# Kernel optimization log

Hardware: AMD Instinct MI355X
Metric: run time of the kernel (lower is better)

The kernel has to match this reference:

```python
import jax, jax.numpy as jnp
import numpy as np

NEG = -1e9


def setup_inputs() -> dict:
    key = jax.random.key(0)
    kq, kk, kv, ke = jax.random.split(key, 4)
    B, H, S, D = 4, 16, 2048, 64
    q = jax.random.normal(kq, (B, H, S, D), dtype=jnp.float32)
    k = jax.random.normal(kk, (B, H, S, D), dtype=jnp.float32)
    v = jax.random.normal(kv, (B, H, S, D), dtype=jnp.float32)
    event_length = jax.random.randint(ke, (B,), 0, S, dtype=jnp.int32)
    return {"q": q, "k": k, "v": v, "event_length": event_length}


def reference(q, k, v, event_length):
    B, H, S, D = q.shape
    scale = jnp.sqrt(jnp.asarray(D, dtype=jnp.float32))
    # [b,h,s,q] scores
    scores = jnp.einsum('bhsd,bhqd->bhsq', q, k) / scale
    idx = jnp.arange(S)
    el = event_length[:, None]  # [B,1]
    valid = idx[None, :] < el   # [B,S]
    # mask[b,s,q] = valid[b,s] & valid[b,q]; broadcast over heads
    mask = (valid[:, None, :, None] & valid[:, None, None, :])  # [B,1,S,S]
    scores = jnp.where(mask, scores, NEG)
    attn = jax.nn.softmax(scores, axis=-1)
    # dropout p=0.0 (eval): identity
    out = jnp.einsum('bhsq,bhqd->bhsd', attn, v)
    return out
```

## Files before the change

kernel.cpp:

```cpp
#include <hip/hip_runtime.h>
#include <hip/hip_bf16.h>


#define SQ 2048
#define DH 64
#define NBH 64
#define TK 64
#define NTILE 32
#define TILE_B 8192
#define PH_B 16384
#define LDE 72
#define LVP 68

typedef __attribute__((ext_vector_type(4))) float f32x4;
typedef __attribute__((ext_vector_type(8))) short bf16x8;
typedef __attribute__((ext_vector_type(4))) unsigned int u32x4;
typedef __attribute__((ext_vector_type(2))) unsigned int u32x2;

#define VMCNT(n) asm volatile("s_waitcnt vmcnt(" #n ")" ::: "memory")
#define RAW_BARRIER() asm volatile("s_barrier" ::: "memory")

__device__ __forceinline__ unsigned int pk2(float lo, float hi) {
    __hip_bfloat162 h = __float22bfloat162_rn(float2{lo, hi});
    union { __hip_bfloat162 h; unsigned int u; } c; c.h = h;
    return c.u;
}

__device__ __forceinline__ float bfu16_to_f(unsigned short s) {
    union { unsigned int u; float f; } c; c.u = ((unsigned int)s) << 16;
    return c.f;
}

__device__ __forceinline__ void async_cp16(const void* g, void* l) {
    __builtin_amdgcn_global_load_lds(
        (const __attribute__((address_space(1))) unsigned int*)g,
        (__attribute__((address_space(3))) unsigned int*)l, 16, 0, 0);
}


__global__ __launch_bounds__(256)
void convkv(const float* __restrict__ K, const float* __restrict__ V,
            const int* __restrict__ EL, float* __restrict__ MV,
            char* __restrict__ Kbt, char* __restrict__ Vbt) {
    const int bh = blockIdx.x >> 5;
    const int kt = blockIdx.x & 31;
    const int k0 = kt * TK;
    const int el = EL[bh >> 4];
    const int t = threadIdx.x;
    const int r  = t >> 2;
    const int dc = t & 3;

    __shared__ short LV[64][LVP];

    {
        const float* vp = V + ((size_t)bh * SQ + k0 + r) * DH + dc * 16;
        f32x4 a = *(const f32x4*)vp;
        f32x4 b = *(const f32x4*)(vp + 4);
        f32x4 c2 = *(const f32x4*)(vp + 8);
        f32x4 d2 = *(const f32x4*)(vp + 12);
        u32x4 w0, w1;
        w0[0] = pk2(a[0], a[1]);  w0[1] = pk2(a[2], a[3]);
        w0[2] = pk2(b[0], b[1]);  w0[3] = pk2(b[2], b[3]);
        w1[0] = pk2(c2[0], c2[1]); w1[1] = pk2(c2[2], c2[3]);
        w1[2] = pk2(d2[0], d2[1]); w1[3] = pk2(d2[2], d2[3]);
        *(u32x4*)&LV[r][dc * 16]     = w0;
        *(u32x4*)&LV[r][dc * 16 + 8] = w1;
    }

    if (k0 < el) {
        const float* kp = K + ((size_t)bh * SQ + k0 + r) * DH + dc * 16;
        f32x4 a = *(const f32x4*)kp;
        f32x4 b = *(const f32x4*)(kp + 4);
        f32x4 c2 = *(const f32x4*)(kp + 8);
        f32x4 d2 = *(const f32x4*)(kp + 12);
        u32x4 w0, w1;
        w0[0] = pk2(a[0], a[1]);  w0[1] = pk2(a[2], a[3]);
        w0[2] = pk2(b[0], b[1]);  w0[3] = pk2(b[2], b[3]);
        w1[0] = pk2(c2[0], c2[1]); w1[1] = pk2(c2[2], c2[3]);
        w1[2] = pk2(d2[0], d2[1]); w1[3] = pk2(d2[2], d2[3]);
        char* kb = Kbt + (size_t)(bh * NTILE + kt) * TILE_B;
        const int fi  = (r >> 4) * 2 + (dc >> 1);
        const int qd0 = (dc & 1) * 2;
        char* d0 = kb + fi * 1024 + qd0 * 256 + (r & 15) * 16;
        *(u32x4*)d0         = w0;
        *(u32x4*)(d0 + 256) = w1;
    }

    __syncthreads();

    const int dd  = t >> 2;
    const int seg = t & 3;
    float msum = 0.f;
    unsigned int wv[8];
    #pragma unroll
    for (int i = 0; i < 8; ++i) {
        const int pos = seg * 16 + 2 * i;
        const int key = (pos & ~31) | ((pos & 4) << 2) | ((pos & 24) >> 1) | (pos & 3);
        const unsigned short s0 = (unsigned short)LV[key][dd];
        const unsigned short s1 = (unsigned short)LV[key + 1][dd];
        msum += bfu16_to_f(s0) + bfu16_to_f(s1);
        wv[i] = (unsigned int)s0 | ((unsigned int)s1 << 16);
    }
    msum += __shfl_xor(msum, 1);
    msum += __shfl_xor(msum, 2);
    if (seg == 0) atomicAdd(&MV[bh * DH + dd], msum * (1.0f / (float)SQ));

    if (k0 < el) {
        char* vbb = Vbt + (size_t)(bh * NTILE + kt) * TILE_B;
        const int fi  = (seg >> 1) * 4 + (dd >> 4);
        const int qd0 = (seg & 1) * 2;
        char* d0 = vbb + fi * 1024 + qd0 * 256 + (dd & 15) * 16;
        u32x4 o0 = {wv[0], wv[1], wv[2], wv[3]};
        u32x4 o1 = {wv[4], wv[5], wv[6], wv[7]};
        *(u32x4*)d0         = o0;
        *(u32x4*)(d0 + 256) = o1;
    }
}

__global__ __launch_bounds__(512, 4)
void flash15(const float* __restrict__ Q, const int* __restrict__ EL,
             const float* __restrict__ MV, float* __restrict__ O,
             const char* __restrict__ Kbt, const char* __restrict__ Vbt) {
    const int t = threadIdx.x;

    {
        const int bh0 = blockIdx.x & (NBH - 1);
        const int qb0 = (blockIdx.x >> 6) * 256;
        const int elb = EL[bh0 >> 4];
        if (qb0 >= elb) {
            float* Op = O + (size_t)bh0 * SQ * DH;
            const int c16 = t & 15, r0 = t >> 4;
            f32x4 mv = *(const f32x4*)(MV + bh0 * DH + c16 * 4);
            #pragma unroll
            for (int i = 0; i < 8; ++i)
                *(f32x4*)(Op + (size_t)(qb0 + r0 + i * 32) * DH + c16 * 4) = mv;
        }
    }

    int ka0 = EL[0], va0 = 0;
    int ka1 = EL[1], va1 = 1;
    int ka2 = EL[2], va2 = 2;
    int ka3 = EL[3], va3 = 3;
    #define CSWAP(x, y) if (ka##x < ka##y) { int tk_ = ka##x, tv_ = va##x; \
        ka##x = ka##y; va##x = va##y; ka##y = tk_; va##y = tv_; }
    CSWAP(0, 1) CSWAP(2, 3) CSWAP(0, 2) CSWAP(1, 3) CSWAP(1, 2)
    #undef CSWAP
    const int c0 = 2 * ((ka0 + 255) >> 8);
    const int c1 = 2 * ((ka1 + 255) >> 8);
    const int c2 = 2 * ((ka2 + 255) >> 8);
    const int c3 = 2 * ((ka3 + 255) >> 8);
    const int nvalid = c0 + c1 + c2 + c3;

    __shared__ char KB[2 * PH_B];
    __shared__ char VB[2 * PH_B];

    const int grp = blockIdx.x & 7;
    const int it  = blockIdx.x >> 3;
    if (it >= nvalid) return;

    int u = it, b, el;
    if (u < c0)             { b = va0; el = ka0; }
    else { u -= c0;
    if (u < c1)             { b = va1; el = ka1; }
    else { u -= c1;
    if (u < c2)             { b = va2; el = ka2; }
    else { u -= c2;           b = va3; el = ka3; } } }
    const int vb_ = (el + 255) >> 8;
    const int hh  = u / vb_;
    const int qt  = u - hh * vb_;
    const int bh  = b * 16 + grp + hh * 8;
    const int qbase = qt * 256;

    const int wq = t >> 6, lane = t & 63, qd = lane >> 4, c = lane & 15;
    const float sc = 0.125f * 1.44269504f;

    const float* Qp = Q + (size_t)bh * SQ * DH;
    float*       Op = O + (size_t)bh * SQ * DH;
    const char*  Kt = Kbt + (size_t)bh * NTILE * TILE_B + t * 16;
    const char*  Vt = Vbt + (size_t)bh * NTILE * TILE_B + t * 16;

    const int nph = (el + 127) >> 7;

    #define STAGE(ph_, s_) {                                                   \
        const char* gk_ = Kt + (size_t)(ph_) * PH_B;                           \
        const char* gv_ = Vt + (size_t)(ph_) * PH_B;                           \
        char* lk_ = KB + (s_) * PH_B + t * 16;                                 \
        char* lv_ = VB + (s_) * PH_B + t * 16;                                 \
        async_cp16(gk_,        lk_);                                           \
        async_cp16(gk_ + 8192, lk_ + 8192);                                    \
        async_cp16(gv_,        lv_);                                           \
        async_cp16(gv_ + 8192, lv_ + 8192);                                    \
    }

    STAGE(0, 0)

    bf16x8 qf[2][2];
    #pragma unroll
    for (int nt = 0; nt < 2; ++nt) {
        const int row = qbase + wq * 32 + nt * 16 + c;
        #pragma unroll
        for (int kc = 0; kc < 2; ++kc) {
            const float* p = Qp + (size_t)row * DH + kc * 32 + qd * 8;
            f32x4 a  = *(const f32x4*)p;
            f32x4 bq = *(const f32x4*)(p + 4);
            u32x4 f;
            f[0] = pk2(a[0] * sc, a[1] * sc);
            f[1] = pk2(a[2] * sc, a[3] * sc);
            f[2] = pk2(bq[0] * sc, bq[1] * sc);
            f[3] = pk2(bq[2] * sc, bq[3] * sc);
            qf[nt][kc] = *(bf16x8*)&f;
        }
    }

    float l_[2] = {0.f, 0.f};
    f32x4 oacc[4][2];
    #pragma unroll
    for (int dt = 0; dt < 4; ++dt) {
        oacc[dt][0] = (f32x4){0.f, 0.f, 0.f, 0.f};
        oacc[dt][1] = (f32x4){0.f, 0.f, 0.f, 0.f};
    }

    for (int ph = 0; ph < nph; ++ph) {
        const int s = ph & 1;

        RAW_BARRIER();
        if (ph + 1 < nph) STAGE(ph + 1, s ^ 1)
        if (ph + 1 < nph) VMCNT(4); else VMCNT(0);
        RAW_BARRIER();

        #pragma unroll
        for (int su = 0; su < 2; ++su) {
            const int k0 = ph * 128 + su * 64;
            if (k0 >= el) break;

            const char* Kb = KB + s * PH_B + su * TILE_B + lane * 16;
            const char* Vb = VB + s * PH_B + su * TILE_B + lane * 16;

            f32x4 st[4][2];
            __builtin_amdgcn_s_setprio(1);
            #pragma unroll
            for (int mt = 0; mt < 4; ++mt) {
                bf16x8 a0 = *(const bf16x8*)(Kb + (mt * 2) * 1024);
                bf16x8 a1 = *(const bf16x8*)(Kb + (mt * 2 + 1) * 1024);
                #pragma unroll
                for (int nt = 0; nt < 2; ++nt) {
                    f32x4 acc = (f32x4){0.f, 0.f, 0.f, 0.f};
                    acc = __builtin_amdgcn_mfma_f32_16x16x32_bf16(a0, qf[nt][0], acc, 0, 0, 0);
                    acc = __builtin_amdgcn_mfma_f32_16x16x32_bf16(a1, qf[nt][1], acc, 0, 0, 0);
                    st[mt][nt] = acc;
                }
            }
            __builtin_amdgcn_s_setprio(0);

            if (k0 + TK > el) {
                #pragma unroll
                for (int mt = 0; mt < 4; ++mt)
                    #pragma unroll
                    for (int r = 0; r < 4; ++r)
                        if (k0 + mt * 16 + qd * 4 + r >= el) {
                            st[mt][0][r] = -1e30f;
                            st[mt][1][r] = -1e30f;
                        }
            }

            u32x4 pw[2][2];
            #pragma unroll
            for (int nt = 0; nt < 2; ++nt) {
                #pragma unroll
                for (int mt = 0; mt < 4; ++mt) {
                    const float p0 = __builtin_amdgcn_exp2f(st[mt][nt][0]);
                    const float p1 = __builtin_amdgcn_exp2f(st[mt][nt][1]);
                    const float p2 = __builtin_amdgcn_exp2f(st[mt][nt][2]);
                    const float p3 = __builtin_amdgcn_exp2f(st[mt][nt][3]);
                    l_[nt] += (p0 + p1) + (p2 + p3);
                    pw[nt][mt >> 1][(mt & 1) * 2]     = pk2(p0, p1);
                    pw[nt][mt >> 1][(mt & 1) * 2 + 1] = pk2(p2, p3);
                }
            }

            __builtin_amdgcn_s_setprio(1);
            #pragma unroll
            for (int kc = 0; kc < 2; ++kc) {
                bf16x8 pb0 = *(bf16x8*)&pw[0][kc];
                bf16x8 pb1 = *(bf16x8*)&pw[1][kc];
                #pragma unroll
                for (int dt = 0; dt < 4; ++dt) {
                    bf16x8 vf = *(const bf16x8*)(Vb + (kc * 4 + dt) * 1024);
                    oacc[dt][0] = __builtin_amdgcn_mfma_f32_16x16x32_bf16(vf, pb0, oacc[dt][0], 0, 0, 0);
                    oacc[dt][1] = __builtin_amdgcn_mfma_f32_16x16x32_bf16(vf, pb1, oacc[dt][1], 0, 0, 0);
                }
            }
            __builtin_amdgcn_s_setprio(0);
        }
    }
    #undef STAGE

    #pragma unroll
    for (int nt = 0; nt < 2; ++nt) {
        l_[nt] += __shfl_xor(l_[nt], 16);
        l_[nt] += __shfl_xor(l_[nt], 32);
    }

    #pragma unroll
    for (int nt = 0; nt < 2; ++nt) {
        const int qrow = qbase + wq * 32 + nt * 16 + c;
        if (qrow < el) {
            const float inv = 1.0f / l_[nt];
            #pragma unroll
            for (int dt = 0; dt < 4; ++dt) {
                f32x4 o = oacc[dt][nt];
                o[0] *= inv; o[1] *= inv; o[2] *= inv; o[3] *= inv;
                *(f32x4*)(Op + (size_t)qrow * DH + dt * 16 + qd * 4) = o;
            }
        } else {
            #pragma unroll
            for (int dt = 0; dt < 4; ++dt)
                *(f32x4*)(Op + (size_t)qrow * DH + dt * 16 + qd * 4) =
                    *(const f32x4*)(MV + bh * DH + dt * 16 + qd * 4);
        }
    }
}


__global__ __launch_bounds__(256)
void meanv_k(const float* __restrict__ V, float* __restrict__ MV) {
    const int bh  = blockIdx.x >> 4;
    const int seg = blockIdx.x & 15;
    const float* vp = V + ((size_t)bh * SQ + (size_t)seg * 128) * DH;
    const int c = threadIdx.x & 15;
    const int r = threadIdx.x >> 4;
    const float* p = vp + (size_t)r * DH + c * 4;
    f32x4 s0 = *(const f32x4*)(p);
    f32x4 s1 = *(const f32x4*)(p + 16 * DH);
    f32x4 s2 = *(const f32x4*)(p + 32 * DH);
    f32x4 s3 = *(const f32x4*)(p + 48 * DH);
    s0 += *(const f32x4*)(p + 64 * DH);
    s1 += *(const f32x4*)(p + 80 * DH);
    s2 += *(const f32x4*)(p + 96 * DH);
    s3 += *(const f32x4*)(p + 112 * DH);
    f32x4 s = (s0 + s1) + (s2 + s3);
    __shared__ f32x4 red[16][16];
    red[r][c] = s;
    __syncthreads();
    if (threadIdx.x < 16) {
        f32x4 a = red[0][threadIdx.x];
        #pragma unroll
        for (int j = 1; j < 16; ++j) a += red[j][threadIdx.x];
        const float inv = 1.0f / (float)SQ;
        atomicAdd(&MV[bh * DH + threadIdx.x * 4 + 0], a[0] * inv);
        atomicAdd(&MV[bh * DH + threadIdx.x * 4 + 1], a[1] * inv);
        atomicAdd(&MV[bh * DH + threadIdx.x * 4 + 2], a[2] * inv);
        atomicAdd(&MV[bh * DH + threadIdx.x * 4 + 3], a[3] * inv);
    }
}

__global__ __launch_bounds__(256, 3)
void flash5(const float* __restrict__ Q, const float* __restrict__ K,
            const float* __restrict__ V, const int* __restrict__ EL,
            const float* __restrict__ MV, float* __restrict__ O,
            int* __restrict__ ticket) {
    const int t = threadIdx.x;
    {
        const int bh0    = blockIdx.x & (NBH - 1);
        const int qbase0 = (blockIdx.x >> 6) * 128;
        const int elb    = EL[bh0 >> 4];
        if (qbase0 >= elb) {
            float* Op = O + (size_t)bh0 * SQ * DH;
            const int c16 = t & 15, r0 = t >> 4;
            f32x4 mv = *(const f32x4*)(MV + bh0 * DH + c16 * 4);
            #pragma unroll
            for (int i = 0; i < 8; ++i)
                *(f32x4*)(Op + (size_t)(qbase0 + r0 + i * 16) * DH + c16 * 4) = mv;
        }
    }

    const int el0 = EL[0], el1 = EL[1], el2 = EL[2], el3 = EL[3];
    const int v0 = (el0 + 127) >> 7, v1 = (el1 + 127) >> 7;
    const int v2 = (el2 + 127) >> 7, v3 = (el3 + 127) >> 7;
    const int n0 = 16 * v0, n1 = n0 + 16 * v1, n2 = n1 + 16 * v2;
    const int nvalid = n2 + 16 * v3;

    __shared__ short Kb[TK][LDE];
    __shared__ short Vt[DH][LDE];
    __shared__ short Pl[4][32][LDE];
    __shared__ int item_s;

    const int wq = t >> 6, lane = t & 63, qd = lane >> 4, c = lane & 15;
    const int ksrow = t >> 2;
    const int ksdc  = t & 3;
    const int vpair = t & 31;
    const int vdg   = t >> 5;

    for (;;) {
        if (t == 0) item_s = atomicAdd(ticket, 1);
        __syncthreads();
        const int it = item_s;
        if (it >= nvalid) break;

        int b, u, vb, el;
        if      (it < n0) { b = 0; u = it;      vb = v0; el = el0; }
        else if (it < n1) { b = 1; u = it - n0; vb = v1; el = el1; }
        else if (it < n2) { b = 2; u = it - n1; vb = v2; el = el2; }
        else              { b = 3; u = it - n2; vb = v3; el = el3; }
        const int head  = u / vb;
        const int qt    = u - head * vb;
        const int bh    = b * 16 + head;
        const int qbase = qt * 128;

        const size_t base = (size_t)bh * SQ * DH;
        const float* Qp = Q + base;
        const float* Kp = K + base;
        const float* Vp = V + base;
        float* Op = O + base;

        const float sc = 0.125f * 1.44269504f;
        bf16x8 qf[2][2];
        #pragma unroll
        for (int nt = 0; nt < 2; ++nt) {
            const int row = qbase + wq * 32 + nt * 16 + c;
            #pragma unroll
            for (int kc = 0; kc < 2; ++kc) {
                const float* p = Qp + (size_t)row * DH + kc * 32 + qd * 8;
                f32x4 a  = *(const f32x4*)p;
                f32x4 bb = *(const f32x4*)(p + 4);
                u32x4 f;
                f[0] = pk2(a[0] * sc, a[1] * sc);
                f[1] = pk2(a[2] * sc, a[3] * sc);
                f[2] = pk2(bb[0] * sc, bb[1] * sc);
                f[3] = pk2(bb[2] * sc, bb[3] * sc);
                qf[nt][kc] = *(bf16x8*)&f;
            }
        }

        float l_[2] = {0.f, 0.f};
        f32x4 oacc[4][2];
        #pragma unroll
        for (int dt = 0; dt < 4; ++dt)
            #pragma unroll
            for (int nt = 0; nt < 2; ++nt)
                oacc[dt][nt] = (f32x4){0.f, 0.f, 0.f, 0.f};

        const int nkt = (el + TK - 1) / TK;

        f32x4 kg0, kg1, kg2, kg3, vg0, vg1, vg2, vg3;
        {
            const float* kp = Kp + (size_t)ksrow * DH + ksdc * 16;
            kg0 = *(const f32x4*)kp;
            kg1 = *(const f32x4*)(kp + 4);
            kg2 = *(const f32x4*)(kp + 8);
            kg3 = *(const f32x4*)(kp + 12);
            const float* vp0 = Vp + (size_t)(2 * vpair) * DH + vdg * 8;
            vg0 = *(const f32x4*)vp0;
            vg1 = *(const f32x4*)(vp0 + 4);
            vg2 = *(const f32x4*)(vp0 + DH);
            vg3 = *(const f32x4*)(vp0 + DH + 4);
        }

        for (int kt = 0; kt < nkt; ++kt) {
            const int k0 = kt * TK;

            __syncthreads();
            {
                u32x4 w0, w1;
                w0[0] = pk2(kg0[0], kg0[1]); w0[1] = pk2(kg0[2], kg0[3]);
                w0[2] = pk2(kg1[0], kg1[1]); w0[3] = pk2(kg1[2], kg1[3]);
                w1[0] = pk2(kg2[0], kg2[1]); w1[1] = pk2(kg2[2], kg2[3]);
                w1[2] = pk2(kg3[0], kg3[1]); w1[3] = pk2(kg3[2], kg3[3]);
                *(u32x4*)&Kb[ksrow][ksdc * 16]     = w0;
                *(u32x4*)&Kb[ksrow][ksdc * 16 + 8] = w1;
            }
            {
                #pragma unroll
                for (int i = 0; i < 4; ++i) {
                    *(unsigned int*)&Vt[vdg * 8 + i][2 * vpair]     = pk2(vg0[i], vg2[i]);
                    *(unsigned int*)&Vt[vdg * 8 + 4 + i][2 * vpair] = pk2(vg1[i], vg3[i]);
                }
            }
            __syncthreads();

            if (kt + 1 < nkt) {
                const int kn = k0 + TK;
                const float* kp = Kp + (size_t)(kn + ksrow) * DH + ksdc * 16;
                kg0 = *(const f32x4*)kp;
                kg1 = *(const f32x4*)(kp + 4);
                kg2 = *(const f32x4*)(kp + 8);
                kg3 = *(const f32x4*)(kp + 12);
                const float* vp0 = Vp + (size_t)(kn + 2 * vpair) * DH + vdg * 8;
                vg0 = *(const f32x4*)vp0;
                vg1 = *(const f32x4*)(vp0 + 4);
                vg2 = *(const f32x4*)(vp0 + DH);
                vg3 = *(const f32x4*)(vp0 + DH + 4);
            }

            f32x4 st[4][2];
            #pragma unroll
            for (int mt = 0; mt < 4; ++mt) {
                bf16x8 a0 = *(const bf16x8*)&Kb[mt * 16 + c][qd * 8];
                bf16x8 a1 = *(const bf16x8*)&Kb[mt * 16 + c][32 + qd * 8];
                #pragma unroll
                for (int nt = 0; nt < 2; ++nt) {
                    f32x4 acc = (f32x4){0.f, 0.f, 0.f, 0.f};
                    acc = __builtin_amdgcn_mfma_f32_16x16x32_bf16(a0, qf[nt][0], acc, 0, 0, 0);
                    acc = __builtin_amdgcn_mfma_f32_16x16x32_bf16(a1, qf[nt][1], acc, 0, 0, 0);
                    st[mt][nt] = acc;
                }
            }

            if (k0 + TK > el) {
                #pragma unroll
                for (int mt = 0; mt < 4; ++mt)
                    #pragma unroll
                    for (int r = 0; r < 4; ++r)
                        if (k0 + mt * 16 + qd * 4 + r >= el) {
                            st[mt][0][r] = -1e30f;
                            st[mt][1][r] = -1e30f;
                        }
            }

            #pragma unroll
            for (int nt = 0; nt < 2; ++nt) {
                #pragma unroll
                for (int mt = 0; mt < 4; ++mt) {
                    const float p0 = exp2f(st[mt][nt][0]);
                    const float p1 = exp2f(st[mt][nt][1]);
                    const float p2 = exp2f(st[mt][nt][2]);
                    const float p3 = exp2f(st[mt][nt][3]);
                    l_[nt] += (p0 + p1) + (p2 + p3);
                    u32x2 pw;
                    pw[0] = pk2(p0, p1);
                    pw[1] = pk2(p2, p3);
                    *(u32x2*)&Pl[wq][nt * 16 + c][mt * 16 + qd * 4] = pw;
                }
            }

            #pragma unroll
            for (int kc = 0; kc < 2; ++kc) {
                bf16x8 pb0 = *(const bf16x8*)&Pl[wq][c][kc * 32 + qd * 8];
                bf16x8 pb1 = *(const bf16x8*)&Pl[wq][16 + c][kc * 32 + qd * 8];
                #pragma unroll
                for (int dt = 0; dt < 4; ++dt) {
                    bf16x8 vf = *(const bf16x8*)&Vt[dt * 16 + c][kc * 32 + qd * 8];
                    oacc[dt][0] = __builtin_amdgcn_mfma_f32_16x16x32_bf16(vf, pb0, oacc[dt][0], 0, 0, 0);
                    oacc[dt][1] = __builtin_amdgcn_mfma_f32_16x16x32_bf16(vf, pb1, oacc[dt][1], 0, 0, 0);
                }
            }
        }

        #pragma unroll
        for (int nt = 0; nt < 2; ++nt) {
            l_[nt] += __shfl_xor(l_[nt], 16);
            l_[nt] += __shfl_xor(l_[nt], 32);
        }

        #pragma unroll
        for (int nt = 0; nt < 2; ++nt) {
            const int row = qbase + wq * 32 + nt * 16 + c;
            if (row < el) {
                const float inv = 1.0f / l_[nt];
                #pragma unroll
                for (int dt = 0; dt < 4; ++dt) {
                    f32x4 o = oacc[dt][nt];
                    o[0] *= inv; o[1] *= inv; o[2] *= inv; o[3] *= inv;
                    *(f32x4*)(Op + (size_t)row * DH + dt * 16 + qd * 4) = o;
                }
            } else {
                #pragma unroll
                for (int dt = 0; dt < 4; ++dt) {
                    f32x4 mv = *(const f32x4*)(MV + bh * DH + dt * 16 + qd * 4);
                    *(f32x4*)(Op + (size_t)row * DH + dt * 16 + qd * 4) = mv;
                }
            }
        }
    }
}


extern "C" void kernel_launch(void* const* d_in, const int* in_sizes, int n_in,
                              void* d_out, int out_size, void* d_ws, size_t ws_size,
                              hipStream_t stream) {
    const float* q  = (const float*)d_in[0];
    const float* k  = (const float*)d_in[1];
    const float* v  = (const float*)d_in[2];
    const int*   el = (const int*)d_in[3];
    float* out = (float*)d_out;

    const size_t kbt_bytes = (size_t)NBH * NTILE * TILE_B;
    const size_t needed    = 65536 + 2 * kbt_bytes;

    if (ws_size >= needed) {
        float* mv  = (float*)d_ws;
        char*  kbt = (char*)d_ws + 65536;
        char*  vbt = kbt + kbt_bytes;

        hipMemsetAsync(d_ws, 0, 65536, stream);
        convkv<<<dim3(NBH * NTILE), dim3(256), 0, stream>>>(k, v, el, mv, kbt, vbt);
        flash15<<<dim3(NBH * (SQ / 256)), dim3(512), 0, stream>>>(q, el, mv, out, kbt, vbt);
    } else {
        float* mv = (float*)d_ws;
        int*   tk = (int*)((char*)d_ws + NBH * DH * sizeof(float));

        hipMemsetAsync(d_ws, 0, NBH * DH * sizeof(float) + 64, stream);
        meanv_k<<<dim3(NBH * 16), dim3(256), 0, stream>>>(v, mv);
        flash5<<<dim3(NBH * (SQ / 128)), dim3(256), 0, stream>>>(q, k, v, el, mv, out, tk);
    }
}
```

Before: 186.1 us.

## Halve block to 256 threads with 64 query rows per wave

Each workgroup now has 4 waves instead of 8, and each wave handles 64 query rows instead of 32. Every K/V fragment loaded from LDS therefore feeds twice as many MFMAs, and fewer waves share each staged K/V tile. The score computation, masking and exp2 are also fused per 16x16 tile so the full score array is never held at once. The cost is a larger accumulator and register footprint (16 output accumulators per lane), lower occupancy (launch bounds 2), and fewer waves available to hide latency.

```diff
diff --git a/kernel.cpp b/kernel.cpp
--- a/kernel.cpp
+++ b/kernel.cpp
@@ -117,8 +117,8 @@
     }
 }
 
-__global__ __launch_bounds__(512, 4)
-void flash15(const float* __restrict__ Q, const int* __restrict__ EL,
+__global__ __launch_bounds__(256, 2)
+void flash17(const float* __restrict__ Q, const int* __restrict__ EL,
              const float* __restrict__ MV, float* __restrict__ O,
              const char* __restrict__ Kbt, const char* __restrict__ Vbt) {
     const int t = threadIdx.x;
@@ -132,8 +132,8 @@
             const int c16 = t & 15, r0 = t >> 4;
             f32x4 mv = *(const f32x4*)(MV + bh0 * DH + c16 * 4);
             #pragma unroll
-            for (int i = 0; i < 8; ++i)
-                *(f32x4*)(Op + (size_t)(qb0 + r0 + i * 32) * DH + c16 * 4) = mv;
+            for (int i = 0; i < 16; ++i)
+                *(f32x4*)(Op + (size_t)(qb0 + r0 + i * 16) * DH + c16 * 4) = mv;
         }
     }
 
@@ -186,18 +186,19 @@
         const char* gv_ = Vt + (size_t)(ph_) * PH_B;                           \
         char* lk_ = KB + (s_) * PH_B + t * 16;                                 \
         char* lv_ = VB + (s_) * PH_B + t * 16;                                 \
-        async_cp16(gk_,        lk_);                                           \
-        async_cp16(gk_ + 8192, lk_ + 8192);                                    \
-        async_cp16(gv_,        lv_);                                           \
-        async_cp16(gv_ + 8192, lv_ + 8192);                                    \
+        _Pragma("unroll")                                                      \
+        for (int j_ = 0; j_ < 4; ++j_) {                                       \
+            async_cp16(gk_ + j_ * 4096, lk_ + j_ * 4096);                      \
+            async_cp16(gv_ + j_ * 4096, lv_ + j_ * 4096);                      \
+        }                                                                      \
     }
 
     STAGE(0, 0)
 
-    bf16x8 qf[2][2];
+    bf16x8 qf[4][2];
     #pragma unroll
-    for (int nt = 0; nt < 2; ++nt) {
-        const int row = qbase + wq * 32 + nt * 16 + c;
+    for (int nt = 0; nt < 4; ++nt) {
+        const int row = qbase + wq * 64 + nt * 16 + c;
         #pragma unroll
         for (int kc = 0; kc < 2; ++kc) {
             const float* p = Qp + (size_t)row * DH + kc * 32 + qd * 8;
@@ -212,20 +213,20 @@
         }
     }
 
-    float l_[2] = {0.f, 0.f};
-    f32x4 oacc[4][2];
+    float l_[4] = {0.f, 0.f, 0.f, 0.f};
+    f32x4 oacc[4][4];
     #pragma unroll
-    for (int dt = 0; dt < 4; ++dt) {
-        oacc[dt][0] = (f32x4){0.f, 0.f, 0.f, 0.f};
-        oacc[dt][1] = (f32x4){0.f, 0.f, 0.f, 0.f};
-    }
+    for (int dt = 0; dt < 4; ++dt)
+        #pragma unroll
+        for (int nt = 0; nt < 4; ++nt)
+            oacc[dt][nt] = (f32x4){0.f, 0.f, 0.f, 0.f};
 
     for (int ph = 0; ph < nph; ++ph) {
         const int s = ph & 1;
 
         RAW_BARRIER();
         if (ph + 1 < nph) STAGE(ph + 1, s ^ 1)
-        if (ph + 1 < nph) VMCNT(4); else VMCNT(0);
+        if (ph + 1 < nph) VMCNT(8); else VMCNT(0);
         RAW_BARRIER();
 
         #pragma unroll
@@ -235,43 +236,29 @@
 
             const char* Kb = KB + s * PH_B + su * TILE_B + lane * 16;
             const char* Vb = VB + s * PH_B + su * TILE_B + lane * 16;
-
-            f32x4 st[4][2];
-            __builtin_amdgcn_s_setprio(1);
+            const bool strad = (k0 + TK > el);
+
+            u32x4 pw[4][2];
             #pragma unroll
             for (int mt = 0; mt < 4; ++mt) {
                 bf16x8 a0 = *(const bf16x8*)(Kb + (mt * 2) * 1024);
                 bf16x8 a1 = *(const bf16x8*)(Kb + (mt * 2 + 1) * 1024);
                 #pragma unroll
-                for (int nt = 0; nt < 2; ++nt) {
-                    f32x4 acc = (f32x4){0.f, 0.f, 0.f, 0.f};
-                    acc = __builtin_amdgcn_mfma_f32_16x16x32_bf16(a0, qf[nt][0], acc, 0, 0, 0);
-                    acc = __builtin_amdgcn_mfma_f32_16x16x32_bf16(a1, qf[nt][1], acc, 0, 0, 0);
-                    st[mt][nt] = acc;
-                }
-            }
-            __builtin_amdgcn_s_setprio(0);
-
-            if (k0 + TK > el) {
-                #pragma unroll
-                for (int mt = 0; mt < 4; ++mt)
-                    #pragma unroll
-                    for (int r = 0; r < 4; ++r)
-                        if (k0 + mt * 16 + qd * 4 + r >= el) {
-                            st[mt][0][r] = -1e30f;
-                            st[mt][1][r] = -1e30f;
-                        }
-            }
-
-            u32x4 pw[2][2];
-            #pragma unroll
-            for (int nt = 0; nt < 2; ++nt) {
-                #pragma unroll
-                for (int mt = 0; mt < 4; ++mt) {
-                    const float p0 = __builtin_amdgcn_exp2f(st[mt][nt][0]);
-                    const float p1 = __builtin_amdgcn_exp2f(st[mt][nt][1]);
-                    const float p2 = __builtin_amdgcn_exp2f(st[mt][nt][2]);
-                    const float p3 = __builtin_amdgcn_exp2f(st[mt][nt][3]);
+                for (int nt = 0; nt < 4; ++nt) {
+                    f32x4 sv = (f32x4){0.f, 0.f, 0.f, 0.f};
+                    __builtin_amdgcn_s_setprio(1);
+                    sv = __builtin_amdgcn_mfma_f32_16x16x32_bf16(a0, qf[nt][0], sv, 0, 0, 0);
+                    sv = __builtin_amdgcn_mfma_f32_16x16x32_bf16(a1, qf[nt][1], sv, 0, 0, 0);
+                    __builtin_amdgcn_s_setprio(0);
+                    if (strad) {
+                        #pragma unroll
+                        for (int r = 0; r < 4; ++r)
+                            if (k0 + mt * 16 + qd * 4 + r >= el) sv[r] = -1e30f;
+                    }
+                    const float p0 = __builtin_amdgcn_exp2f(sv[0]);
+                    const float p1 = __builtin_amdgcn_exp2f(sv[1]);
+                    const float p2 = __builtin_amdgcn_exp2f(sv[2]);
+                    const float p3 = __builtin_amdgcn_exp2f(sv[3]);
                     l_[nt] += (p0 + p1) + (p2 + p3);
                     pw[nt][mt >> 1][(mt & 1) * 2]     = pk2(p0, p1);
                     pw[nt][mt >> 1][(mt & 1) * 2 + 1] = pk2(p2, p3);
@@ -281,13 +268,14 @@
             __builtin_amdgcn_s_setprio(1);
             #pragma unroll
             for (int kc = 0; kc < 2; ++kc) {
-                bf16x8 pb0 = *(bf16x8*)&pw[0][kc];
-                bf16x8 pb1 = *(bf16x8*)&pw[1][kc];
                 #pragma unroll
                 for (int dt = 0; dt < 4; ++dt) {
                     bf16x8 vf = *(const bf16x8*)(Vb + (kc * 4 + dt) * 1024);
-                    oacc[dt][0] = __builtin_amdgcn_mfma_f32_16x16x32_bf16(vf, pb0, oacc[dt][0], 0, 0, 0);
-                    oacc[dt][1] = __builtin_amdgcn_mfma_f32_16x16x32_bf16(vf, pb1, oacc[dt][1], 0, 0, 0);
+                    #pragma unroll
+                    for (int nt = 0; nt < 4; ++nt) {
+                        bf16x8 pb = *(bf16x8*)&pw[nt][kc];
+                        oacc[dt][nt] = __builtin_amdgcn_mfma_f32_16x16x32_bf16(vf, pb, oacc[dt][nt], 0, 0, 0);
+                    }
                 }
             }
             __builtin_amdgcn_s_setprio(0);
@@ -296,14 +284,14 @@
     #undef STAGE
 
     #pragma unroll
-    for (int nt = 0; nt < 2; ++nt) {
+    for (int nt = 0; nt < 4; ++nt) {
         l_[nt] += __shfl_xor(l_[nt], 16);
         l_[nt] += __shfl_xor(l_[nt], 32);
     }
 
     #pragma unroll
-    for (int nt = 0; nt < 2; ++nt) {
-        const int qrow = qbase + wq * 32 + nt * 16 + c;
+    for (int nt = 0; nt < 4; ++nt) {
+        const int qrow = qbase + wq * 64 + nt * 16 + c;
         if (qrow < el) {
             const float inv = 1.0f / l_[nt];
             #pragma unroll
@@ -594,7 +582,7 @@
 
         hipMemsetAsync(d_ws, 0, 65536, stream);
         convkv<<<dim3(NBH * NTILE), dim3(256), 0, stream>>>(k, v, el, mv, kbt, vbt);
-        flash15<<<dim3(NBH * (SQ / 256)), dim3(512), 0, stream>>>(q, el, mv, out, kbt, vbt);
+        flash17<<<dim3(NBH * (SQ / 256)), dim3(256), 0, stream>>>(q, el, mv, out, kbt, vbt);
     } else {
         float* mv = (float*)d_ws;
         int*   tk = (int*)((char*)d_ws + NBH * DH * sizeof(float));
```

After: 192.9 us. +3.6%, slower.

## Split attention key range across blocks with atomic accumulation and finalize pass

Applied to the files above, without the earlier changes.

Adds a flash18 kernel that divides each query tile's key range into segments of 8 key tiles, each handled by its own block. When there are several segments, blocks add unnormalised outputs and row sums into the zeroed output and a workspace buffer using atomics. A new finalize kernel then normalises the rows and fills masked rows with the mean of V. The aim is more parallelism and better load balance across blocks when the valid lengths differ. The cost is a memset of the whole output, per-element float atomics, and an extra full read and write of the output.

```diff
diff --git a/kernel.cpp b/kernel.cpp
--- a/kernel.cpp
+++ b/kernel.cpp
@@ -9,6 +9,7 @@
 #define NTILE 32
 #define TILE_B 8192
 #define PH_B 16384
+#define PHSEG 8
 #define LDE 72
 #define LVP 68
 
@@ -36,7 +37,6 @@
         (const __attribute__((address_space(1))) unsigned int*)g,
         (__attribute__((address_space(3))) unsigned int*)l, 16, 0, 0);
 }
-
 
 __global__ __launch_bounds__(256)
 void convkv(const float* __restrict__ K, const float* __restrict__ V,
@@ -118,24 +118,13 @@
 }
 
 __global__ __launch_bounds__(512, 4)
-void flash15(const float* __restrict__ Q, const int* __restrict__ EL,
-             const float* __restrict__ MV, float* __restrict__ O,
+void flash18(const float* __restrict__ Q, const int* __restrict__ EL,
+             float* __restrict__ O, float* __restrict__ Lacc,
              const char* __restrict__ Kbt, const char* __restrict__ Vbt) {
-    const int t = threadIdx.x;
-
-    {
-        const int bh0 = blockIdx.x & (NBH - 1);
-        const int qb0 = (blockIdx.x >> 6) * 256;
-        const int elb = EL[bh0 >> 4];
-        if (qb0 >= elb) {
-            float* Op = O + (size_t)bh0 * SQ * DH;
-            const int c16 = t & 15, r0 = t >> 4;
-            f32x4 mv = *(const f32x4*)(MV + bh0 * DH + c16 * 4);
-            #pragma unroll
-            for (int i = 0; i < 8; ++i)
-                *(f32x4*)(Op + (size_t)(qb0 + r0 + i * 32) * DH + c16 * 4) = mv;
-        }
-    }
+    const int blk = blockIdx.x;
+    const int grp = blk & 7;
+    const int it  = (blk >> 3) & 63;
+    const int sgi = blk >> 9;
 
     int ka0 = EL[0], va0 = 0;
     int ka1 = EL[1], va1 = 1;
@@ -150,12 +139,6 @@
     const int c2 = 2 * ((ka2 + 255) >> 8);
     const int c3 = 2 * ((ka3 + 255) >> 8);
     const int nvalid = c0 + c1 + c2 + c3;
-
-    __shared__ char KB[2 * PH_B];
-    __shared__ char VB[2 * PH_B];
-
-    const int grp = blockIdx.x & 7;
-    const int it  = blockIdx.x >> 3;
     if (it >= nvalid) return;
 
     int u = it, b, el;
@@ -171,6 +154,16 @@
     const int bh  = b * 16 + grp + hh * 8;
     const int qbase = qt * 256;
 
+    const int nph  = (el + 63) >> 6;
+    const int nseg = (nph + PHSEG - 1) / PHSEG;
+    if (sgi >= nseg) return;
+    const int p0 = sgi * PHSEG;
+    const int p1 = (p0 + PHSEG < nph) ? p0 + PHSEG : nph;
+
+    __shared__ char KB[2 * TILE_B];
+    __shared__ char VB[2 * TILE_B];
+
+    const int t = threadIdx.x;
     const int wq = t >> 6, lane = t & 63, qd = lane >> 4, c = lane & 15;
     const float sc = 0.125f * 1.44269504f;
 
@@ -178,21 +171,15 @@
     float*       Op = O + (size_t)bh * SQ * DH;
     const char*  Kt = Kbt + (size_t)bh * NTILE * TILE_B + t * 16;
     const char*  Vt = Vbt + (size_t)bh * NTILE * TILE_B + t * 16;
-
-    const int nph = (el + 127) >> 7;
+    char* const  kdst = KB + wq * 1024;
+    char* const  vdst = VB + wq * 1024;
 
     #define STAGE(ph_, s_) {                                                   \
-        const char* gk_ = Kt + (size_t)(ph_) * PH_B;                           \
-        const char* gv_ = Vt + (size_t)(ph_) * PH_B;                           \
-        char* lk_ = KB + (s_) * PH_B + t * 16;                                 \
-        char* lv_ = VB + (s_) * PH_B + t * 16;                                 \
-        async_cp16(gk_,        lk_);                                           \
-        async_cp16(gk_ + 8192, lk_ + 8192);                                    \
-        async_cp16(gv_,        lv_);                                           \
-        async_cp16(gv_ + 8192, lv_ + 8192);                                    \
-    }
-
-    STAGE(0, 0)
+        async_cp16(Kt + (size_t)(ph_) * TILE_B, kdst + (s_) * TILE_B);         \
+        async_cp16(Vt + (size_t)(ph_) * TILE_B, vdst + (s_) * TILE_B);         \
+    }
+
+    STAGE(p0, 0)
 
     bf16x8 qf[2][2];
     #pragma unroll
@@ -220,9 +207,246 @@
         oacc[dt][1] = (f32x4){0.f, 0.f, 0.f, 0.f};
     }
 
+    for (int ph = p0; ph < p1; ++ph) {
+        const int s = (ph - p0) & 1;
+
+        RAW_BARRIER();
+        if (ph + 1 < p1) STAGE(ph + 1, s ^ 1)
+        if (ph + 1 < p1) VMCNT(2); else VMCNT(0);
+        RAW_BARRIER();
+
+        const char* Kb = KB + s * TILE_B + lane * 16;
+        const char* Vb = VB + s * TILE_B + lane * 16;
+
+        f32x4 st[4][2];
+        __builtin_amdgcn_s_setprio(1);
+        #pragma unroll
+        for (int mt = 0; mt < 4; ++mt) {
+            bf16x8 a0 = *(const bf16x8*)(Kb + (mt * 2) * 1024);
+            bf16x8 a1 = *(const bf16x8*)(Kb + (mt * 2 + 1) * 1024);
+            #pragma unroll
+            for (int nt = 0; nt < 2; ++nt) {
+                f32x4 acc = (f32x4){0.f, 0.f, 0.f, 0.f};
+                acc = __builtin_amdgcn_mfma_f32_16x16x32_bf16(a0, qf[nt][0], acc, 0, 0, 0);
+                acc = __builtin_amdgcn_mfma_f32_16x16x32_bf16(a1, qf[nt][1], acc, 0, 0, 0);
+                st[mt][nt] = acc;
+            }
+        }
+        __builtin_amdgcn_s_setprio(0);
+
+        const int k0 = ph * TK;
+        if (k0 + TK > el) {
+            #pragma unroll
+            for (int mt = 0; mt < 4; ++mt)
+                #pragma unroll
+                for (int r = 0; r < 4; ++r)
+                    if (k0 + mt * 16 + qd * 4 + r >= el) {
+                        st[mt][0][r] = -1e30f;
+                        st[mt][1][r] = -1e30f;
+                    }
+        }
+
+        u32x4 pw[2][2];
+        #pragma unroll
+        for (int nt = 0; nt < 2; ++nt) {
+            #pragma unroll
+            for (int mt = 0; mt < 4; ++mt) {
+                const float p0f = __builtin_amdgcn_exp2f(st[mt][nt][0]);
+                const float p1f = __builtin_amdgcn_exp2f(st[mt][nt][1]);
+                const float p2f = __builtin_amdgcn_exp2f(st[mt][nt][2]);
+                const float p3f = __builtin_amdgcn_exp2f(st[mt][nt][3]);
+                l_[nt] += (p0f + p1f) + (p2f + p3f);
+                pw[nt][mt >> 1][(mt & 1) * 2]     = pk2(p0f, p1f);
+                pw[nt][mt >> 1][(mt & 1) * 2 + 1] = pk2(p2f, p3f);
+            }
+        }
+
+        __builtin_amdgcn_s_setprio(1);
+        #pragma unroll
+        for (int kc = 0; kc < 2; ++kc) {
+            bf16x8 pb0 = *(bf16x8*)&pw[0][kc];
+            bf16x8 pb1 = *(bf16x8*)&pw[1][kc];
+            #pragma unroll
+            for (int dt = 0; dt < 4; ++dt) {
+                bf16x8 vf = *(const bf16x8*)(Vb + (kc * 4 + dt) * 1024);
+                oacc[dt][0] = __builtin_amdgcn_mfma_f32_16x16x32_bf16(vf, pb0, oacc[dt][0], 0, 0, 0);
+                oacc[dt][1] = __builtin_amdgcn_mfma_f32_16x16x32_bf16(vf, pb1, oacc[dt][1], 0, 0, 0);
+            }
+        }
+        __builtin_amdgcn_s_setprio(0);
+    }
+    #undef STAGE
+
+    #pragma unroll
+    for (int nt = 0; nt < 2; ++nt) {
+        l_[nt] += __shfl_xor(l_[nt], 16);
+        l_[nt] += __shfl_xor(l_[nt], 32);
+    }
+
+    if (nseg == 1) {
+        #pragma unroll
+        for (int nt = 0; nt < 2; ++nt) {
+            const int qrow = qbase + wq * 32 + nt * 16 + c;
+            if (qrow < el) {
+                const float inv = 1.0f / l_[nt];
+                #pragma unroll
+                for (int dt = 0; dt < 4; ++dt) {
+                    f32x4 o = oacc[dt][nt];
+                    o[0] *= inv; o[1] *= inv; o[2] *= inv; o[3] *= inv;
+                    *(f32x4*)(Op + (size_t)qrow * DH + dt * 16 + qd * 4) = o;
+                }
+            }
+        }
+    } else {
+        #pragma unroll
+        for (int nt = 0; nt < 2; ++nt) {
+            const int qrow = qbase + wq * 32 + nt * 16 + c;
+            if (qrow < el) {
+                float* op = Op + (size_t)qrow * DH + qd * 4;
+                #pragma unroll
+                for (int dt = 0; dt < 4; ++dt) {
+                    atomicAdd(op + dt * 16 + 0, oacc[dt][nt][0]);
+                    atomicAdd(op + dt * 16 + 1, oacc[dt][nt][1]);
+                    atomicAdd(op + dt * 16 + 2, oacc[dt][nt][2]);
+                    atomicAdd(op + dt * 16 + 3, oacc[dt][nt][3]);
+                }
+                if (qd == 0) atomicAdd(&Lacc[bh * SQ + qrow], l_[nt]);
+            }
+        }
+    }
+}
+
+__global__ __launch_bounds__(256)
+void finalize(const int* __restrict__ EL, const float* __restrict__ Lacc,
+              const float* __restrict__ MV, float* __restrict__ O) {
+    const int bh = blockIdx.x >> 4;
+    const int ch = blockIdx.x & 15;
+    const int el = EL[bh >> 4];
+    const int c16 = threadIdx.x & 15, r0 = threadIdx.x >> 4;
+    float* Op = O + (size_t)bh * SQ * DH;
+    const float* Lp = Lacc + bh * SQ;
+    f32x4 mv = *(const f32x4*)(MV + bh * DH + c16 * 4);
+    #pragma unroll
+    for (int i = 0; i < 8; ++i) {
+        const int row = ch * 128 + r0 + i * 16;
+        if (row >= el) {
+            *(f32x4*)(Op + (size_t)row * DH + c16 * 4) = mv;
+        } else {
+            const float l = Lp[row];
+            if (l != 0.f) {
+                const float inv = 1.0f / l;
+                f32x4 o = *(const f32x4*)(Op + (size_t)row * DH + c16 * 4);
+                o[0] *= inv; o[1] *= inv; o[2] *= inv; o[3] *= inv;
+                *(f32x4*)(Op + (size_t)row * DH + c16 * 4) = o;
+            }
+        }
+    }
+}
+
+__global__ __launch_bounds__(512, 4)
+void flash15(const float* __restrict__ Q, const int* __restrict__ EL,
+             const float* __restrict__ MV, float* __restrict__ O,
+             const char* __restrict__ Kbt, const char* __restrict__ Vbt) {
+    const int t = threadIdx.x;
+    {
+        const int bh0 = blockIdx.x & (NBH - 1);
+        const int qb0 = (blockIdx.x >> 6) * 256;
+        const int elb = EL[bh0 >> 4];
+        if (qb0 >= elb) {
+            float* Op = O + (size_t)bh0 * SQ * DH;
+            const int c16 = t & 15, r0 = t >> 4;
+            f32x4 mv = *(const f32x4*)(MV + bh0 * DH + c16 * 4);
+            #pragma unroll
+            for (int i = 0; i < 8; ++i)
+                *(f32x4*)(Op + (size_t)(qb0 + r0 + i * 32) * DH + c16 * 4) = mv;
+        }
+    }
+
+    int ka0 = EL[0], va0 = 0;
+    int ka1 = EL[1], va1 = 1;
+    int ka2 = EL[2], va2 = 2;
+    int ka3 = EL[3], va3 = 3;
+    #define CSWAP(x, y) if (ka##x < ka##y) { int tk_ = ka##x, tv_ = va##x; \
+        ka##x = ka##y; va##x = va##y; ka##y = tk_; va##y = tv_; }
+    CSWAP(0, 1) CSWAP(2, 3) CSWAP(0, 2) CSWAP(1, 3) CSWAP(1, 2)
+    #undef CSWAP
+    const int c0 = 2 * ((ka0 + 255) >> 8);
+    const int c1 = 2 * ((ka1 + 255) >> 8);
+    const int c2 = 2 * ((ka2 + 255) >> 8);
+    const int c3 = 2 * ((ka3 + 255) >> 8);
+    const int nvalid = c0 + c1 + c2 + c3;
+
+    __shared__ char KB[2 * PH_B];
+    __shared__ char VB[2 * PH_B];
+
+    const int grp = blockIdx.x & 7;
+    const int it  = blockIdx.x >> 3;
+    if (it >= nvalid) return;
+
+    int u = it, b, el;
+    if (u < c0)             { b = va0; el = ka0; }
+    else { u -= c0;
+    if (u < c1)             { b = va1; el = ka1; }
+    else { u -= c1;
+    if (u < c2)             { b = va2; el = ka2; }
+    else { u -= c2;           b = va3; el = ka3; } } }
+    const int vb_ = (el + 255) >> 8;
+    const int hh  = u / vb_;
+    const int qt  = u - hh * vb_;
+    const int bh  = b * 16 + grp + hh * 8;
+    const int qbase = qt * 256;
+
+    const int wq = t >> 6, lane = t & 63, qd = lane >> 4, c = lane & 15;
+    const float sc = 0.125f * 1.44269504f;
+
+    const float* Qp = Q + (size_t)bh * SQ * DH;
+    float*       Op = O + (size_t)bh * SQ * DH;
+    const char*  Kt = Kbt + (size_t)bh * NTILE * TILE_B + t * 16;
+    const char*  Vt = Vbt + (size_t)bh * NTILE * TILE_B + t * 16;
+
+    const int nph = (el + 127) >> 7;
+
+    #define STAGE(ph_, s_) {                                                   \
+        const char* gk_ = Kt + (size_t)(ph_) * PH_B;                           \
+        const char* gv_ = Vt + (size_t)(ph_) * PH_B;                           \
+        char* lk_ = KB + (s_) * PH_B + t * 16;                                 \
+        char* lv_ = VB + (s_) * PH_B + t * 16;                                 \
+        async_cp16(gk_,        lk_);                                           \
+        async_cp16(gk_ + 8192, lk_ + 8192);                                    \
+        async_cp16(gv_,        lv_);                                           \
+        async_cp16(gv_ + 8192, lv_ + 8192);                                    \
+    }
+
+    STAGE(0, 0)
+
+    bf16x8 qf[2][2];
+    #pragma unroll
+    for (int nt = 0; nt < 2; ++nt) {
+        const int row = qbase + wq * 32 + nt * 16 + c;
+        #pragma unroll
+        for (int kc = 0; kc < 2; ++kc) {
+            const float* p = Qp + (size_t)row * DH + kc * 32 + qd * 8;
+            f32x4 a  = *(const f32x4*)p;
+            f32x4 bq = *(const f32x4*)(p + 4);
+            u32x4 f;
+            f[0] = pk2(a[0] * sc, a[1] * sc);
+            f[1] = pk2(a[2] * sc, a[3] * sc);
+            f[2] = pk2(bq[0] * sc, bq[1] * sc);
+            f[3] = pk2(bq[2] * sc, bq[3] * sc);
+            qf[nt][kc] = *(bf16x8*)&f;
+        }
+    }
+
+    float l_[2] = {0.f, 0.f};
+    f32x4 oacc[4][2];
+    #pragma unroll
+    for (int dt = 0; dt < 4; ++dt) {
+        oacc[dt][0] = (f32x4){0.f, 0.f, 0.f, 0.f};
+        oacc[dt][1] = (f32x4){0.f, 0.f, 0.f, 0.f};
+    }
+
     for (int ph = 0; ph < nph; ++ph) {
         const int s = ph & 1;
-
         RAW_BARRIER();
         if (ph + 1 < nph) STAGE(ph + 1, s ^ 1)
         if (ph + 1 < nph) VMCNT(4); else VMCNT(0);
@@ -320,7 +544,6 @@
         }
     }
 }
-
 
 __global__ __launch_bounds__(256)
 void meanv_k(const float* __restrict__ V, float* __restrict__ MV) {
@@ -585,9 +808,22 @@
     float* out = (float*)d_out;
 
     const size_t kbt_bytes = (size_t)NBH * NTILE * TILE_B;
-    const size_t needed    = 65536 + 2 * kbt_bytes;
-
-    if (ws_size >= needed) {
+    const size_t lacc_bytes = (size_t)NBH * SQ * sizeof(float);
+    const size_t needed15  = 65536 + 2 * kbt_bytes;
+    const size_t needed18  = 65536 + lacc_bytes + 2 * kbt_bytes;
+
+    if (ws_size >= needed18) {
+        float* mv   = (float*)d_ws;
+        float* lacc = (float*)((char*)d_ws + 65536);
+        char*  kbt  = (char*)d_ws + 65536 + lacc_bytes;
+        char*  vbt  = kbt + kbt_bytes;
+
+        hipMemsetAsync(d_ws, 0, 65536 + lacc_bytes, stream);
+        hipMemsetAsync(d_out, 0, (size_t)out_size, stream);
+        convkv<<<dim3(NBH * NTILE), dim3(256), 0, stream>>>(k, v, el, mv, kbt, vbt);
+        flash18<<<dim3(8 * 64 * 4), dim3(512), 0, stream>>>(q, el, out, lacc, kbt, vbt);
+        finalize<<<dim3(NBH * 16), dim3(256), 0, stream>>>(el, lacc, mv, out);
+    } else if (ws_size >= needed15) {
         float* mv  = (float*)d_ws;
         char*  kbt = (char*)d_ws + 65536;
         char*  vbt = kbt + kbt_bytes;
```

Measured after the change: 339.1 us. +82.2%, slower.
